# Performance work log

Measured on AMD Instinct MI355X. Metric: run time of the kernel, lower is better.

The kernel has to match this reference:

```python
import jax, jax.numpy as jnp
import numpy as np

N_NODES = 50000
N_EDGES = 800000
IN_DIM = 128
EDGE_DIM = 128
OUT_DIM = 128
N_AGG = 4          # mean, max, min, std
N_SCALE = 3        # identity, amplification, attenuation
AVG_D_LOG = float(np.log(17.0))  # log(avg_degree + 1), PNA avg_d['log']
EPS = 1e-5


def setup_inputs() -> dict:
    key = jax.random.key(0)
    ks = jax.random.split(key, 10)
    pre_in = 2 * IN_DIM + EDGE_DIM                      # pretrans input dim
    post_in = (N_AGG * N_SCALE + 1) * IN_DIM            # posttrans input dim
    return {
        "node_feat": jax.random.normal(ks[0], (N_NODES, IN_DIM), jnp.float32),
        "edge_feat": jax.random.normal(ks[1], (N_EDGES, EDGE_DIM), jnp.float32),
        "w_pre": jax.random.normal(ks[2], (pre_in, IN_DIM), jnp.float32) * (1.0 / np.sqrt(pre_in)),
        "b_pre": jnp.zeros((IN_DIM,), jnp.float32),
        "w_post1": jax.random.normal(ks[3], (post_in, OUT_DIM), jnp.float32) * (1.0 / np.sqrt(post_in)),
        "b_post1": jnp.zeros((OUT_DIM,), jnp.float32),
        "w_post2": jax.random.normal(ks[4], (OUT_DIM, OUT_DIM), jnp.float32) * (1.0 / np.sqrt(OUT_DIM)),
        "b_post2": jnp.zeros((OUT_DIM,), jnp.float32),
        "src": jax.random.randint(ks[5], (N_EDGES,), 0, N_NODES, jnp.int32),
        "dst": jax.random.randint(ks[6], (N_EDGES,), 0, N_NODES, jnp.int32),
    }


def reference(node_feat, edge_feat, w_pre, b_pre, w_post1, b_post1,
              w_post2, b_post2, src, dst):
    n = node_feat.shape[0]
    # --- pretrans over edges: MLP(cat[src_h, dst_h, edge_feat]) -> message ---
    z = jnp.concatenate([node_feat[src], node_feat[dst], edge_feat], axis=-1)  # [E, 2d+de]
    msg = jax.nn.relu(z @ w_pre + b_pre)                                       # [E, d]

    # --- multi-aggregator scatter-reduce per destination node ---
    ones = jnp.ones((msg.shape[0],), msg.dtype)
    deg = jax.ops.segment_sum(ones, dst, num_segments=n)                       # [N]
    d_safe = jnp.maximum(deg, 1.0)[:, None]
    has_nb = (deg > 0)[:, None]

    s1 = jax.ops.segment_sum(msg, dst, num_segments=n)
    s2 = jax.ops.segment_sum(msg * msg, dst, num_segments=n)
    a_mean = s1 / d_safe
    a_var = jax.nn.relu(s2 / d_safe - a_mean * a_mean)
    a_std = jnp.sqrt(a_var + EPS)
    a_max = jnp.where(has_nb, jax.ops.segment_max(msg, dst, num_segments=n), 0.0)
    a_min = jnp.where(has_nb, jax.ops.segment_min(msg, dst, num_segments=n), 0.0)
    agg = jnp.concatenate([a_mean, a_max, a_min, a_std], axis=-1)              # [N, 4d]

    # --- degree scalers: identity, amplification, attenuation ---
    logd = jnp.log(deg + 1.0)[:, None]
    amp = agg * (logd / AVG_D_LOG)
    att = agg * (AVG_D_LOG / jnp.maximum(logd, EPS))
    h = jnp.concatenate([node_feat, agg, amp, att], axis=-1)                   # [N, 13d]

    # --- posttrans MLP + residual ---
    h1 = jax.nn.relu(h @ w_post1 + b_post1)
    out = h1 @ w_post2 + b_post2 + node_feat                                   # residual (in_dim == out_dim)
    return out
```

## Files before the change

### kernel.cpp

```cpp
#include <hip/hip_runtime.h>
#include <math.h>

#define N_NODES 50000
#define N_EDGES 800000
#define D 128
#define AVG_D_LOG 2.833213344056216f
#define EPS 1e-5f

typedef __attribute__((ext_vector_type(8))) short bf16x8;
typedef __attribute__((ext_vector_type(4))) float f32x4;

__device__ __forceinline__ unsigned short f2bf(float x) {
    unsigned u = __float_as_uint(x);
    u += 0x7fffu + ((u >> 16) & 1u);
    return (unsigned short)(u >> 16);
}
__device__ __forceinline__ unsigned pk2bf(float a, float b) {
    return (unsigned)f2bf(a) | ((unsigned)f2bf(b) << 16);
}
__device__ __forceinline__ float bf2f(unsigned short u) {
    return __uint_as_float(((unsigned)u) << 16);
}

__global__ void k_init(int* hist, float* s1, float* s2, float* mx, float* mn) {
    size_t stride = (size_t)gridDim.x * blockDim.x;
    size_t i0 = (size_t)blockIdx.x * blockDim.x + threadIdx.x;
    const size_t ND4 = (size_t)N_NODES * D / 4;
    float4 z4 = {0.f, 0.f, 0.f, 0.f};
    int4 inf4 = {0x7f800000, 0x7f800000, 0x7f800000, 0x7f800000};
    for (size_t t = i0; t < ND4; t += stride) {
        ((float4*)s1)[t] = z4; ((float4*)s2)[t] = z4; ((float4*)mx)[t] = z4;
        ((int4*)mn)[t] = inf4;
    }
    for (size_t t = i0; t < N_NODES; t += stride) hist[t] = 0;
}

__global__ void k_hist(const int* __restrict__ dst, int* hist) {
    int e = blockIdx.x * blockDim.x + threadIdx.x;
    if (e < N_EDGES) atomicAdd(&hist[dst[e]], 1);
}

__global__ void k_scan(const int* __restrict__ hist, int* cursor) {
    __shared__ int part[256];
    __shared__ int base_s[256];
    int t = threadIdx.x;
    const int chunk = (N_NODES + 255) / 256;
    int lo = t * chunk;
    int hi = lo + chunk; if (hi > N_NODES) hi = N_NODES;
    int s = 0;
    for (int i = lo; i < hi; ++i) s += hist[i];
    part[t] = s;
    __syncthreads();
    if (t == 0) {
        int run = 0;
        for (int i = 0; i < 256; ++i) { base_s[i] = run; run += part[i]; }
    }
    __syncthreads();
    int run = base_s[t];
    for (int i = lo; i < hi; ++i) { cursor[i] = run; run += hist[i]; }
}

__global__ void k_scatter(const int* __restrict__ dst, int* cursor, int* perm) {
    int e = blockIdx.x * blockDim.x + threadIdx.x;
    if (e < N_EDGES) {
        int pos = atomicAdd(&cursor[dst[e]], 1);
        perm[pos] = e;
    }
}

__global__ void k_prepT(const float* __restrict__ w, unsigned short* __restrict__ wT, int K) {
    int idx = blockIdx.x * blockDim.x + threadIdx.x;
    if (idx >= K * D) return;
    int k = idx >> 7, c = idx & 127;
    wT[(size_t)c * K + k] = f2bf(w[idx]);
}

__global__ __launch_bounds__(256) void k_pretrans(
    const float* __restrict__ nf, const float* __restrict__ ef,
    const unsigned short* __restrict__ wpT, const float* __restrict__ bp,
    const int* __restrict__ src, const int* __restrict__ dst,
    const int* __restrict__ perm,
    float* s1, float* s2, float* mx, float* mn)
{
    __shared__ __align__(16) char smem[24576];
    __shared__ int pidx[64], sidx[64], didx[64];
    __shared__ int seg_start[65], seg_dst[64];
    __shared__ int nseg_s;
    __shared__ float sb[128];

    int t = threadIdx.x;
    int e0 = blockIdx.x * 64;
    if (t < 64) {
        int pe = perm[e0 + t];
        pidx[t] = pe; sidx[t] = src[pe]; didx[t] = dst[pe];
    }
    if (t < 128) sb[t] = bp[t];
    __syncthreads();

    int w  = t >> 6;
    int l  = t & 63;
    int lr = l & 15;
    int lg = l >> 4;

    f32x4 acc[2][4];
    #pragma unroll
    for (int i = 0; i < 2; ++i)
        #pragma unroll
        for (int j = 0; j < 4; ++j) acc[i][j] = (f32x4){0.f, 0.f, 0.f, 0.f};

    uint4  pw0, pw1, pw2, pw3;
    float4 pz0, pz1, pz2, pz3;

#define ZROW(NC, e) ((NC) < 2 ? nf + (size_t)sidx[e] * D : \
                     (NC) < 4 ? nf + (size_t)didx[e] * D : \
                                ef + (size_t)pidx[e] * D)

#define PF(NC) do { \
    { int g = t;       int c = g >> 3, j = g & 7;  pw0 = *(const uint4*)(wpT + (size_t)c * 384 + (NC) * 64 + j * 8); } \
    { int g = t + 256; int c = g >> 3, j = g & 7;  pw1 = *(const uint4*)(wpT + (size_t)c * 384 + (NC) * 64 + j * 8); } \
    { int g = t + 512; int c = g >> 3, j = g & 7;  pw2 = *(const uint4*)(wpT + (size_t)c * 384 + (NC) * 64 + j * 8); } \
    { int g = t + 768; int c = g >> 3, j = g & 7;  pw3 = *(const uint4*)(wpT + (size_t)c * 384 + (NC) * 64 + j * 8); } \
    { int g = t;       int e = g >> 4, q = g & 15; pz0 = *(const float4*)(ZROW(NC, e) + (((NC) & 1) * 64) + q * 4); } \
    { int g = t + 256; int e = g >> 4, q = g & 15; pz1 = *(const float4*)(ZROW(NC, e) + (((NC) & 1) * 64) + q * 4); } \
    { int g = t + 512; int e = g >> 4, q = g & 15; pz2 = *(const float4*)(ZROW(NC, e) + (((NC) & 1) * 64) + q * 4); } \
    { int g = t + 768; int e = g >> 4, q = g & 15; pz3 = *(const float4*)(ZROW(NC, e) + (((NC) & 1) * 64) + q * 4); } \
} while (0)

#define WR() do { \
    { int g = t;       int c = g >> 3, j = g & 7;  *(uint4*)(smem + c * 128 + ((j * 16) ^ ((c & 7) << 4))) = pw0; } \
    { int g = t + 256; int c = g >> 3, j = g & 7;  *(uint4*)(smem + c * 128 + ((j * 16) ^ ((c & 7) << 4))) = pw1; } \
    { int g = t + 512; int c = g >> 3, j = g & 7;  *(uint4*)(smem + c * 128 + ((j * 16) ^ ((c & 7) << 4))) = pw2; } \
    { int g = t + 768; int c = g >> 3, j = g & 7;  *(uint4*)(smem + c * 128 + ((j * 16) ^ ((c & 7) << 4))) = pw3; } \
    { int g = t;       int e = g >> 4, q = g & 15; uint2 hv = { pk2bf(pz0.x, pz0.y), pk2bf(pz0.z, pz0.w) }; \
      *(uint2*)(smem + 16384 + e * 128 + ((q * 8) ^ ((e & 7) << 4))) = hv; } \
    { int g = t + 256; int e = g >> 4, q = g & 15; uint2 hv = { pk2bf(pz1.x, pz1.y), pk2bf(pz1.z, pz1.w) }; \
      *(uint2*)(smem + 16384 + e * 128 + ((q * 8) ^ ((e & 7) << 4))) = hv; } \
    { int g = t + 512; int e = g >> 4, q = g & 15; uint2 hv = { pk2bf(pz2.x, pz2.y), pk2bf(pz2.z, pz2.w) }; \
      *(uint2*)(smem + 16384 + e * 128 + ((q * 8) ^ ((e & 7) << 4))) = hv; } \
    { int g = t + 768; int e = g >> 4, q = g & 15; uint2 hv = { pk2bf(pz3.x, pz3.y), pk2bf(pz3.z, pz3.w) }; \
      *(uint2*)(smem + 16384 + e * 128 + ((q * 8) ^ ((e & 7) << 4))) = hv; } \
} while (0)

#define MM() do { \
    _Pragma("unroll") \
    for (int ks = 0; ks < 2; ++ks) { \
        bf16x8 afr[2], bfr[4]; \
        int kb = ks * 64 + lg * 16; \
        _Pragma("unroll") \
        for (int cf = 0; cf < 2; ++cf) { \
            int c = w * 32 + cf * 16 + lr; \
            afr[cf] = *(const bf16x8*)(smem + c * 128 + (kb ^ ((c & 7) << 4))); \
        } \
        _Pragma("unroll") \
        for (int eb = 0; eb < 4; ++eb) { \
            int e = eb * 16 + lr; \
            bfr[eb] = *(const bf16x8*)(smem + 16384 + e * 128 + (kb ^ ((e & 7) << 4))); \
        } \
        _Pragma("unroll") \
        for (int cf = 0; cf < 2; ++cf) \
            _Pragma("unroll") \
            for (int eb = 0; eb < 4; ++eb) \
                acc[cf][eb] = __builtin_amdgcn_mfma_f32_16x16x32_bf16( \
                    afr[cf], bfr[eb], acc[cf][eb], 0, 0, 0); \
    } \
} while (0)

    PF(0);
    WR(); PF(1); __syncthreads(); MM(); __syncthreads();
    WR(); PF(2); __syncthreads(); MM(); __syncthreads();
    WR(); PF(3); __syncthreads(); MM(); __syncthreads();
    WR(); PF(4); __syncthreads(); MM(); __syncthreads();
    WR(); PF(5); __syncthreads(); MM(); __syncthreads();
    WR();        __syncthreads(); MM(); __syncthreads();

#undef ZROW
#undef PF
#undef WR
#undef MM

    #pragma unroll
    for (int cf = 0; cf < 2; ++cf)
        #pragma unroll
        for (int eb = 0; eb < 4; ++eb) {
            int e  = eb * 16 + lr;
            int c0 = w * 32 + cf * 16 + lg * 4;
            float v0 = fmaxf(acc[cf][eb][0] + sb[c0 + 0], 0.f);
            float v1 = fmaxf(acc[cf][eb][1] + sb[c0 + 1], 0.f);
            float v2 = fmaxf(acc[cf][eb][2] + sb[c0 + 2], 0.f);
            float v3 = fmaxf(acc[cf][eb][3] + sb[c0 + 3], 0.f);
            uint2 mv = { pk2bf(v0, v1), pk2bf(v2, v3) };
            *(uint2*)(smem + e * 256 + ((c0 * 2) ^ ((e & 7) << 4))) = mv;
        }
    if (t == 0) {
        int ns = 0;
        for (int e = 0; e < 64; ++e) {
            if (e == 0 || didx[e] != didx[e - 1]) { seg_dst[ns] = didx[e]; seg_start[ns] = e; ++ns; }
        }
        seg_start[ns] = 64; nseg_s = ns;
    }
    __syncthreads();
    int nseg = nseg_s;
    for (int idx = t; idx < nseg * D; idx += 256) {
        int sg = idx >> 7, c = idx & 127;
        int eb2 = seg_start[sg], ee = seg_start[sg + 1];
        float s = 0.f, q = 0.f, vmax = 0.f, vmin = __int_as_float(0x7f800000);
        for (int e = eb2; e < ee; ++e) {
            float v = bf2f(*(const unsigned short*)(smem + e * 256 + ((c * 2) ^ ((e & 7) << 4))));
            s += v; q += v * v;
            vmax = fmaxf(vmax, v); vmin = fminf(vmin, v);
        }
        size_t base = (size_t)seg_dst[sg] * D + c;
        atomicAdd(&s1[base], s);
        atomicAdd(&s2[base], q);
        atomicMax((int*)&mx[base], __float_as_int(vmax));
        atomicMin((int*)&mn[base], __float_as_int(vmin));
    }
}

__global__ void k_finalize(float* s1, float* s2, float* mx, float* mn,
                           const int* __restrict__ hist, float* scal) {
    size_t idx = (size_t)blockIdx.x * blockDim.x + threadIdx.x;
    if (idx >= (size_t)N_NODES * D) return;
    int n = (int)(idx >> 7);
    int c = (int)(idx & 127);
    float dg = (float)hist[n];
    float ds = fmaxf(dg, 1.f);
    float m  = s1[idx] / ds;
    float var = fmaxf(s2[idx] / ds - m * m, 0.f);
    float sd  = sqrtf(var + EPS);
    bool nb = dg > 0.f;
    s1[idx] = m;
    mx[idx] = nb ? mx[idx] : 0.f;
    mn[idx] = nb ? mn[idx] : 0.f;
    s2[idx] = sd;
    if (c == 0) {
        float logd = logf(dg + 1.f);
        scal[2 * n]     = logd / AVG_D_LOG;
        scal[2 * n + 1] = AVG_D_LOG / fmaxf(logd, EPS);
    }
}

__global__ __launch_bounds__(256, 3) void k_post1(
    const float* __restrict__ nf,
    const float* __restrict__ amean, const float* __restrict__ amax,
    const float* __restrict__ amin,  const float* __restrict__ astd,
    const float* __restrict__ scal,
    const unsigned short* __restrict__ w1T, const float* __restrict__ b1,
    unsigned short* __restrict__ h1bf)
{
    __shared__ __align__(16) char smem[49152];
    __shared__ float samp[64], satt[64], sb[128];

    int t = threadIdx.x;
    int n0 = blockIdx.x * 64;
    if (t < 64) {
        int n = n0 + t;
        samp[t] = (n < N_NODES) ? scal[2 * n] : 0.f;
        satt[t] = (n < N_NODES) ? scal[2 * n + 1] : 0.f;
    }
    if (t < 128) sb[t] = b1[t];
    __syncthreads();

    int w  = t >> 6, l = t & 63, lr = l & 15, lg = l >> 4;
    f32x4 acc[2][4];
    #pragma unroll
    for (int i = 0; i < 2; ++i)
        #pragma unroll
        for (int j = 0; j < 4; ++j) acc[i][j] = (f32x4){0.f, 0.f, 0.f, 0.f};

    for (int chunk = 0; chunk < 13; ++chunk) {
        #pragma unroll
        for (int p = 0; p < 8; ++p) {
            int g = t + 256 * p;
            int c = g >> 4, j = g & 15;
            uint4 wv = *(const uint4*)(w1T + (size_t)c * 1664 + chunk * 128 + j * 8);
            *(uint4*)(smem + c * 256 + ((j * 16) ^ ((c & 7) << 4))) = wv;
        }
        const float* base;
        int r;
        if (chunk == 0) { base = nf; r = 0; }
        else {
            int b = (chunk - 1) & 3;
            r = (chunk - 1) >> 2;
            base = (b == 0) ? amean : (b == 1) ? amax : (b == 2) ? amin : astd;
        }
        #pragma unroll
        for (int p = 0; p < 8; ++p) {
            int g = t + 256 * p;
            int e = g >> 5, q = g & 31;
            int n = n0 + e;
            float4 fv = {0.f, 0.f, 0.f, 0.f};
            if (n < N_NODES) {
                fv = *(const float4*)(base + (size_t)n * D + q * 4);
                if (r == 1) { float sc = samp[e]; fv.x *= sc; fv.y *= sc; fv.z *= sc; fv.w *= sc; }
                else if (r == 2) { float sc = satt[e]; fv.x *= sc; fv.y *= sc; fv.z *= sc; fv.w *= sc; }
            }
            uint2 hv = { pk2bf(fv.x, fv.y), pk2bf(fv.z, fv.w) };
            *(uint2*)(smem + 32768 + e * 256 + ((q * 8) ^ ((e & 7) << 4))) = hv;
        }
        __syncthreads();
        #pragma unroll
        for (int ks = 0; ks < 4; ++ks) {
            bf16x8 afr[2], bfr[4];
            int kb = ks * 64 + lg * 16;
            #pragma unroll
            for (int cf = 0; cf < 2; ++cf) {
                int c = w * 32 + cf * 16 + lr;
                afr[cf] = *(const bf16x8*)(smem + c * 256 + (kb ^ ((c & 7) << 4)));
            }
            #pragma unroll
            for (int eb = 0; eb < 4; ++eb) {
                int e = eb * 16 + lr;
                bfr[eb] = *(const bf16x8*)(smem + 32768 + e * 256 + (kb ^ ((e & 7) << 4)));
            }
            #pragma unroll
            for (int cf = 0; cf < 2; ++cf)
                #pragma unroll
                for (int eb = 0; eb < 4; ++eb)
                    acc[cf][eb] = __builtin_amdgcn_mfma_f32_16x16x32_bf16(
                        afr[cf], bfr[eb], acc[cf][eb], 0, 0, 0);
        }
        __syncthreads();
    }

    #pragma unroll
    for (int cf = 0; cf < 2; ++cf)
        #pragma unroll
        for (int eb = 0; eb < 4; ++eb) {
            int n = n0 + eb * 16 + lr;
            if (n < N_NODES) {
                int c0 = w * 32 + cf * 16 + lg * 4;
                float v0 = fmaxf(acc[cf][eb][0] + sb[c0 + 0], 0.f);
                float v1 = fmaxf(acc[cf][eb][1] + sb[c0 + 1], 0.f);
                float v2 = fmaxf(acc[cf][eb][2] + sb[c0 + 2], 0.f);
                float v3 = fmaxf(acc[cf][eb][3] + sb[c0 + 3], 0.f);
                uint2 hv = { pk2bf(v0, v1), pk2bf(v2, v3) };
                *(uint2*)(h1bf + (size_t)n * D + c0) = hv;
            }
        }
}

__global__ __launch_bounds__(256, 3) void k_post2(
    const unsigned short* __restrict__ h1bf, const unsigned short* __restrict__ w2T,
    const float* __restrict__ b2, const float* __restrict__ nf,
    float* __restrict__ out)
{
    __shared__ __align__(16) char smem[49152];
    __shared__ float sb[128];

    int t = threadIdx.x;
    int n0 = blockIdx.x * 64;
    if (t < 128) sb[t] = b2[t];

    int w  = t >> 6, l = t & 63, lr = l & 15, lg = l >> 4;
    f32x4 acc[2][4];
    #pragma unroll
    for (int i = 0; i < 2; ++i)
        #pragma unroll
        for (int j = 0; j < 4; ++j) acc[i][j] = (f32x4){0.f, 0.f, 0.f, 0.f};

    #pragma unroll
    for (int p = 0; p < 8; ++p) {
        int g = t + 256 * p;
        int c = g >> 4, j = g & 15;
        uint4 wv = *(const uint4*)(w2T + (size_t)c * 128 + j * 8);
        *(uint4*)(smem + c * 256 + ((j * 16) ^ ((c & 7) << 4))) = wv;
    }
    #pragma unroll
    for (int p = 0; p < 4; ++p) {
        int g = t + 256 * p;
        int e = g >> 4, j = g & 15;
        int n = n0 + e;
        uint4 hv = {0u, 0u, 0u, 0u};
        if (n < N_NODES) hv = *(const uint4*)(h1bf + (size_t)n * D + j * 8);
        *(uint4*)(smem + 32768 + e * 256 + ((j * 16) ^ ((e & 7) << 4))) = hv;
    }
    __syncthreads();
    #pragma unroll
    for (int ks = 0; ks < 4; ++ks) {
        bf16x8 afr[2], bfr[4];
        int kb = ks * 64 + lg * 16;
        #pragma unroll
        for (int cf = 0; cf < 2; ++cf) {
            int c = w * 32 + cf * 16 + lr;
            afr[cf] = *(const bf16x8*)(smem + c * 256 + (kb ^ ((c & 7) << 4)));
        }
        #pragma unroll
        for (int eb = 0; eb < 4; ++eb) {
            int e = eb * 16 + lr;
            bfr[eb] = *(const bf16x8*)(smem + 32768 + e * 256 + (kb ^ ((e & 7) << 4)));
        }
        #pragma unroll
        for (int cf = 0; cf < 2; ++cf)
            #pragma unroll
            for (int eb = 0; eb < 4; ++eb)
                acc[cf][eb] = __builtin_amdgcn_mfma_f32_16x16x32_bf16(
                    afr[cf], bfr[eb], acc[cf][eb], 0, 0, 0);
    }

    #pragma unroll
    for (int cf = 0; cf < 2; ++cf)
        #pragma unroll
        for (int eb = 0; eb < 4; ++eb) {
            int n = n0 + eb * 16 + lr;
            if (n < N_NODES) {
                int c0 = w * 32 + cf * 16 + lg * 4;
                float4 rv = *(const float4*)(nf + (size_t)n * D + c0);
                float4 ov = { acc[cf][eb][0] + sb[c0 + 0] + rv.x,
                              acc[cf][eb][1] + sb[c0 + 1] + rv.y,
                              acc[cf][eb][2] + sb[c0 + 2] + rv.z,
                              acc[cf][eb][3] + sb[c0 + 3] + rv.w };
                *(float4*)(out + (size_t)n * D + c0) = ov;
            }
        }
}

extern "C" void kernel_launch(void* const* d_in, const int* in_sizes, int n_in,
                              void* d_out, int out_size, void* d_ws, size_t ws_size,
                              hipStream_t stream) {
    const float* nf = (const float*)d_in[0];
    const float* ef = (const float*)d_in[1];
    const float* wp = (const float*)d_in[2];
    const float* bp = (const float*)d_in[3];
    const float* w1 = (const float*)d_in[4];
    const float* b1 = (const float*)d_in[5];
    const float* w2 = (const float*)d_in[6];
    const float* b2 = (const float*)d_in[7];
    const int* src  = (const int*)d_in[8];
    const int* dst  = (const int*)d_in[9];
    float* out = (float*)d_out;

    const size_t ND = (size_t)N_NODES * D;
    float* ws     = (float*)d_ws;
    int*   hist   = (int*)ws;
    int*   cursor = hist + 50048;
    int*   perm   = cursor + 50048;
    unsigned short* wpT = (unsigned short*)(perm + N_EDGES);
    unsigned short* w1T = wpT + 49152;
    unsigned short* w2T = w1T + 212992;
    float* s1     = (float*)(w2T + 16384);
    float* s2     = s1 + ND;
    float* mx     = s2 + ND;
    float* mn     = mx + ND;
    float* scal   = mn + ND;
    unsigned short* h1bf = (unsigned short*)(scal + 100096);

    hipLaunchKernelGGL(k_init, dim3(2048), dim3(256), 0, stream, hist, s1, s2, mx, mn);
    hipLaunchKernelGGL(k_hist, dim3((N_EDGES + 255) / 256), dim3(256), 0, stream, dst, hist);
    hipLaunchKernelGGL(k_scan, dim3(1), dim3(256), 0, stream, hist, cursor);
    hipLaunchKernelGGL(k_scatter, dim3((N_EDGES + 255) / 256), dim3(256), 0, stream, dst, cursor, perm);
    hipLaunchKernelGGL(k_prepT, dim3(192), dim3(256), 0, stream, wp, wpT, 384);
    hipLaunchKernelGGL(k_prepT, dim3(832), dim3(256), 0, stream, w1, w1T, 1664);
    hipLaunchKernelGGL(k_prepT, dim3(64),  dim3(256), 0, stream, w2, w2T, 128);
    hipLaunchKernelGGL(k_pretrans, dim3(N_EDGES / 64), dim3(256), 0, stream,
                       nf, ef, wpT, bp, src, dst, perm, s1, s2, mx, mn);
    hipLaunchKernelGGL(k_finalize, dim3((unsigned)((ND + 255) / 256)), dim3(256), 0, stream,
                       s1, s2, mx, mn, hist, scal);
    hipLaunchKernelGGL(k_post1, dim3((N_NODES + 63) / 64), dim3(256), 0, stream,
                       nf, s1, mx, mn, s2, scal, w1T, b1, h1bf);
    hipLaunchKernelGGL(k_post2, dim3((N_NODES + 63) / 64), dim3(256), 0, stream,
                       h1bf, w2T, b2, nf, out);
}
```

Baseline: 608.8 us.

## Replace atomic scatter aggregation with CSR segmented reduction over stored messages

The pretrans kernel now writes bf16 messages, sorted by destination, to a global buffer instead of doing atomic segment reductions. A new per-node kernel walks each node's contiguous CSR range and computes sum, sum of squares, max, min and the degree scalers in one pass. This removes the float atomics, the large init of the s1/s2/mx/mn arrays and the separate finalize pass. In exchange it adds a write and re-read of a 200MB message buffer, and it falls back to the old path when the workspace is too small.

```diff
diff --git a/kernel.cpp b/kernel.cpp
--- a/kernel.cpp
+++ b/kernel.cpp
@@ -33,6 +33,11 @@
         ((int4*)mn)[t] = inf4;
     }
     for (size_t t = i0; t < N_NODES; t += stride) hist[t] = 0;
+}
+
+__global__ void k_init_h(int* hist) {
+    int i = blockIdx.x * blockDim.x + threadIdx.x;
+    if (i < N_NODES) hist[i] = 0;
 }
 
 __global__ void k_hist(const int* __restrict__ dst, int* hist) {
@@ -75,46 +80,9 @@
     wT[(size_t)c * K + k] = f2bf(w[idx]);
 }
 
-__global__ __launch_bounds__(256) void k_pretrans(
-    const float* __restrict__ nf, const float* __restrict__ ef,
-    const unsigned short* __restrict__ wpT, const float* __restrict__ bp,
-    const int* __restrict__ src, const int* __restrict__ dst,
-    const int* __restrict__ perm,
-    float* s1, float* s2, float* mx, float* mn)
-{
-    __shared__ __align__(16) char smem[24576];
-    __shared__ int pidx[64], sidx[64], didx[64];
-    __shared__ int seg_start[65], seg_dst[64];
-    __shared__ int nseg_s;
-    __shared__ float sb[128];
-
-    int t = threadIdx.x;
-    int e0 = blockIdx.x * 64;
-    if (t < 64) {
-        int pe = perm[e0 + t];
-        pidx[t] = pe; sidx[t] = src[pe]; didx[t] = dst[pe];
-    }
-    if (t < 128) sb[t] = bp[t];
-    __syncthreads();
-
-    int w  = t >> 6;
-    int l  = t & 63;
-    int lr = l & 15;
-    int lg = l >> 4;
-
-    f32x4 acc[2][4];
-    #pragma unroll
-    for (int i = 0; i < 2; ++i)
-        #pragma unroll
-        for (int j = 0; j < 4; ++j) acc[i][j] = (f32x4){0.f, 0.f, 0.f, 0.f};
-
-    uint4  pw0, pw1, pw2, pw3;
-    float4 pz0, pz1, pz2, pz3;
-
 #define ZROW(NC, e) ((NC) < 2 ? nf + (size_t)sidx[e] * D : \
                      (NC) < 4 ? nf + (size_t)didx[e] * D : \
                                 ef + (size_t)pidx[e] * D)
-
 #define PF(NC) do { \
     { int g = t;       int c = g >> 3, j = g & 7;  pw0 = *(const uint4*)(wpT + (size_t)c * 384 + (NC) * 64 + j * 8); } \
     { int g = t + 256; int c = g >> 3, j = g & 7;  pw1 = *(const uint4*)(wpT + (size_t)c * 384 + (NC) * 64 + j * 8); } \
@@ -125,7 +93,6 @@
     { int g = t + 512; int e = g >> 4, q = g & 15; pz2 = *(const float4*)(ZROW(NC, e) + (((NC) & 1) * 64) + q * 4); } \
     { int g = t + 768; int e = g >> 4, q = g & 15; pz3 = *(const float4*)(ZROW(NC, e) + (((NC) & 1) * 64) + q * 4); } \
 } while (0)
-
 #define WR() do { \
     { int g = t;       int c = g >> 3, j = g & 7;  *(uint4*)(smem + c * 128 + ((j * 16) ^ ((c & 7) << 4))) = pw0; } \
     { int g = t + 256; int c = g >> 3, j = g & 7;  *(uint4*)(smem + c * 128 + ((j * 16) ^ ((c & 7) << 4))) = pw1; } \
@@ -140,7 +107,6 @@
     { int g = t + 768; int e = g >> 4, q = g & 15; uint2 hv = { pk2bf(pz3.x, pz3.y), pk2bf(pz3.z, pz3.w) }; \
       *(uint2*)(smem + 16384 + e * 128 + ((q * 8) ^ ((e & 7) << 4))) = hv; } \
 } while (0)
-
 #define MM() do { \
     _Pragma("unroll") \
     for (int ks = 0; ks < 2; ++ks) { \
@@ -165,6 +131,40 @@
     } \
 } while (0)
 
+__global__ __launch_bounds__(256) void k_pretrans_g(
+    const float* __restrict__ nf, const float* __restrict__ ef,
+    const unsigned short* __restrict__ wpT, const float* __restrict__ bp,
+    const int* __restrict__ src, const int* __restrict__ dst,
+    const int* __restrict__ perm,
+    unsigned short* __restrict__ msgG)
+{
+    __shared__ __align__(16) char smem[24576];
+    __shared__ int pidx[64], sidx[64], didx[64];
+    __shared__ float sb[128];
+
+    int t = threadIdx.x;
+    int e0 = blockIdx.x * 64;
+    if (t < 64) {
+        int pe = perm[e0 + t];
+        pidx[t] = pe; sidx[t] = src[pe]; didx[t] = dst[pe];
+    }
+    if (t < 128) sb[t] = bp[t];
+    __syncthreads();
+
+    int w  = t >> 6;
+    int l  = t & 63;
+    int lr = l & 15;
+    int lg = l >> 4;
+
+    f32x4 acc[2][4];
+    #pragma unroll
+    for (int i = 0; i < 2; ++i)
+        #pragma unroll
+        for (int j = 0; j < 4; ++j) acc[i][j] = (f32x4){0.f, 0.f, 0.f, 0.f};
+
+    uint4  pw0, pw1, pw2, pw3;
+    float4 pz0, pz1, pz2, pz3;
+
     PF(0);
     WR(); PF(1); __syncthreads(); MM(); __syncthreads();
     WR(); PF(2); __syncthreads(); MM(); __syncthreads();
@@ -172,11 +172,6 @@
     WR(); PF(4); __syncthreads(); MM(); __syncthreads();
     WR(); PF(5); __syncthreads(); MM(); __syncthreads();
     WR();        __syncthreads(); MM(); __syncthreads();
-
-#undef ZROW
-#undef PF
-#undef WR
-#undef MM
 
     #pragma unroll
     for (int cf = 0; cf < 2; ++cf)
@@ -191,6 +186,117 @@
             uint2 mv = { pk2bf(v0, v1), pk2bf(v2, v3) };
             *(uint2*)(smem + e * 256 + ((c0 * 2) ^ ((e & 7) << 4))) = mv;
         }
+    __syncthreads();
+    #pragma unroll
+    for (int p = 0; p < 4; ++p) {
+        int e = (t >> 4) + p * 16;
+        int q = t & 15;
+        uint4 v = *(const uint4*)(smem + e * 256 + q * 16);
+        int qq = q ^ (e & 7);
+        *(uint4*)(msgG + (size_t)(e0 + e) * D + qq * 8) = v;
+    }
+}
+
+__global__ __launch_bounds__(256) void k_agg(
+    const unsigned short* __restrict__ msgG,
+    const int* __restrict__ cursor, const int* __restrict__ hist,
+    float* __restrict__ s1, float* __restrict__ s2,
+    float* __restrict__ mx, float* __restrict__ mn, float* __restrict__ scal)
+{
+    int t = threadIdx.x;
+    int n = blockIdx.x * 4 + (t >> 6);
+    int tl = t & 63;
+    int deg = hist[n];
+    int re  = cursor[n];
+    int rs  = re - deg;
+
+    float sum0 = 0.f, sum1 = 0.f, sq0 = 0.f, sq1 = 0.f;
+    float mx0 = -3.402823e38f, mx1 = -3.402823e38f;
+    float mn0 =  3.402823e38f, mn1 =  3.402823e38f;
+    const uint* mg = (const uint*)msgG;
+    for (int e = 0; e < deg; ++e) {
+        uint v = mg[(size_t)(rs + e) * 64 + tl];
+        float a = bf2f((unsigned short)(v & 0xffff));
+        float b = bf2f((unsigned short)(v >> 16));
+        sum0 += a; sum1 += b; sq0 += a * a; sq1 += b * b;
+        mx0 = fmaxf(mx0, a); mx1 = fmaxf(mx1, b);
+        mn0 = fminf(mn0, a); mn1 = fminf(mn1, b);
+    }
+    float dg = (float)deg;
+    float ds = fmaxf(dg, 1.f);
+    bool nb = deg > 0;
+    float m0 = sum0 / ds, m1 = sum1 / ds;
+    float sd0 = sqrtf(fmaxf(sq0 / ds - m0 * m0, 0.f) + EPS);
+    float sd1 = sqrtf(fmaxf(sq1 / ds - m1 * m1, 0.f) + EPS);
+    size_t base = (size_t)n * D + tl * 2;
+    *(float2*)&s1[base] = (float2){m0, m1};
+    *(float2*)&s2[base] = (float2){sd0, sd1};
+    *(float2*)&mx[base] = (float2){nb ? mx0 : 0.f, nb ? mx1 : 0.f};
+    *(float2*)&mn[base] = (float2){nb ? mn0 : 0.f, nb ? mn1 : 0.f};
+    if (tl == 0) {
+        float logd = logf(dg + 1.f);
+        scal[2 * n]     = logd / AVG_D_LOG;
+        scal[2 * n + 1] = AVG_D_LOG / fmaxf(logd, EPS);
+    }
+}
+
+__global__ __launch_bounds__(256) void k_pretrans(
+    const float* __restrict__ nf, const float* __restrict__ ef,
+    const unsigned short* __restrict__ wpT, const float* __restrict__ bp,
+    const int* __restrict__ src, const int* __restrict__ dst,
+    const int* __restrict__ perm,
+    float* s1, float* s2, float* mx, float* mn)
+{
+    __shared__ __align__(16) char smem[24576];
+    __shared__ int pidx[64], sidx[64], didx[64];
+    __shared__ int seg_start[65], seg_dst[64];
+    __shared__ int nseg_s;
+    __shared__ float sb[128];
+
+    int t = threadIdx.x;
+    int e0 = blockIdx.x * 64;
+    if (t < 64) {
+        int pe = perm[e0 + t];
+        pidx[t] = pe; sidx[t] = src[pe]; didx[t] = dst[pe];
+    }
+    if (t < 128) sb[t] = bp[t];
+    __syncthreads();
+
+    int w  = t >> 6;
+    int l  = t & 63;
+    int lr = l & 15;
+    int lg = l >> 4;
+
+    f32x4 acc[2][4];
+    #pragma unroll
+    for (int i = 0; i < 2; ++i)
+        #pragma unroll
+        for (int j = 0; j < 4; ++j) acc[i][j] = (f32x4){0.f, 0.f, 0.f, 0.f};
+
+    uint4  pw0, pw1, pw2, pw3;
+    float4 pz0, pz1, pz2, pz3;
+
+    PF(0);
+    WR(); PF(1); __syncthreads(); MM(); __syncthreads();
+    WR(); PF(2); __syncthreads(); MM(); __syncthreads();
+    WR(); PF(3); __syncthreads(); MM(); __syncthreads();
+    WR(); PF(4); __syncthreads(); MM(); __syncthreads();
+    WR(); PF(5); __syncthreads(); MM(); __syncthreads();
+    WR();        __syncthreads(); MM(); __syncthreads();
+
+    #pragma unroll
+    for (int cf = 0; cf < 2; ++cf)
+        #pragma unroll
+        for (int eb = 0; eb < 4; ++eb) {
+            int e  = eb * 16 + lr;
+            int c0 = w * 32 + cf * 16 + lg * 4;
+            float v0 = fmaxf(acc[cf][eb][0] + sb[c0 + 0], 0.f);
+            float v1 = fmaxf(acc[cf][eb][1] + sb[c0 + 1], 0.f);
+            float v2 = fmaxf(acc[cf][eb][2] + sb[c0 + 2], 0.f);
+            float v3 = fmaxf(acc[cf][eb][3] + sb[c0 + 3], 0.f);
+            uint2 mv = { pk2bf(v0, v1), pk2bf(v2, v3) };
+            *(uint2*)(smem + e * 256 + ((c0 * 2) ^ ((e & 7) << 4))) = mv;
+        }
     if (t == 0) {
         int ns = 0;
         for (int e = 0; e < 64; ++e) {
@@ -216,6 +322,11 @@
         atomicMin((int*)&mn[base], __float_as_int(vmin));
     }
 }
+
+#undef ZROW
+#undef PF
+#undef WR
+#undef MM
 
 __global__ void k_finalize(float* s1, float* s2, float* mx, float* mn,
                            const int* __restrict__ hist, float* scal) {
@@ -431,31 +542,55 @@
     float* out = (float*)d_out;
 
     const size_t ND = (size_t)N_NODES * D;
-    float* ws     = (float*)d_ws;
-    int*   hist   = (int*)ws;
+    char* wsb = (char*)d_ws;
+    int*   hist   = (int*)wsb;
     int*   cursor = hist + 50048;
     int*   perm   = cursor + 50048;
     unsigned short* wpT = (unsigned short*)(perm + N_EDGES);
     unsigned short* w1T = wpT + 49152;
     unsigned short* w2T = w1T + 212992;
-    float* s1     = (float*)(w2T + 16384);
+    unsigned short* msgG = w2T + 16384;
+    const size_t MSG_SH = (size_t)N_EDGES * D;
+    float* s1     = (float*)(msgG + MSG_SH);
     float* s2     = s1 + ND;
     float* mx     = s2 + ND;
     float* mn     = mx + ND;
     float* scal   = mn + ND;
     unsigned short* h1bf = (unsigned short*)(scal + 100096);
-
-    hipLaunchKernelGGL(k_init, dim3(2048), dim3(256), 0, stream, hist, s1, s2, mx, mn);
+    size_t need_csr = (size_t)((char*)(h1bf + ND) - wsb);
+
+    bool use_csr = ws_size >= need_csr;
+    if (!use_csr) {
+        s1   = (float*)(w2T + 16384);
+        s2   = s1 + ND;
+        mx   = s2 + ND;
+        mn   = mx + ND;
+        scal = mn + ND;
+        h1bf = (unsigned short*)(scal + 100096);
+    }
+
+    if (use_csr) {
+        hipLaunchKernelGGL(k_init_h, dim3((N_NODES + 255) / 256), dim3(256), 0, stream, hist);
+    } else {
+        hipLaunchKernelGGL(k_init, dim3(2048), dim3(256), 0, stream, hist, s1, s2, mx, mn);
+    }
     hipLaunchKernelGGL(k_hist, dim3((N_EDGES + 255) / 256), dim3(256), 0, stream, dst, hist);
     hipLaunchKernelGGL(k_scan, dim3(1), dim3(256), 0, stream, hist, cursor);
     hipLaunchKernelGGL(k_scatter, dim3((N_EDGES + 255) / 256), dim3(256), 0, stream, dst, cursor, perm);
     hipLaunchKernelGGL(k_prepT, dim3(192), dim3(256), 0, stream, wp, wpT, 384);
     hipLaunchKernelGGL(k_prepT, dim3(832), dim3(256), 0, stream, w1, w1T, 1664);
     hipLaunchKernelGGL(k_prepT, dim3(64),  dim3(256), 0, stream, w2, w2T, 128);
-    hipLaunchKernelGGL(k_pretrans, dim3(N_EDGES / 64), dim3(256), 0, stream,
-                       nf, ef, wpT, bp, src, dst, perm, s1, s2, mx, mn);
-    hipLaunchKernelGGL(k_finalize, dim3((unsigned)((ND + 255) / 256)), dim3(256), 0, stream,
-                       s1, s2, mx, mn, hist, scal);
+    if (use_csr) {
+        hipLaunchKernelGGL(k_pretrans_g, dim3(N_EDGES / 64), dim3(256), 0, stream,
+                           nf, ef, wpT, bp, src, dst, perm, msgG);
+        hipLaunchKernelGGL(k_agg, dim3(N_NODES / 4), dim3(256), 0, stream,
+                           msgG, cursor, hist, s1, s2, mx, mn, scal);
+    } else {
+        hipLaunchKernelGGL(k_pretrans, dim3(N_EDGES / 64), dim3(256), 0, stream,
+                           nf, ef, wpT, bp, src, dst, perm, s1, s2, mx, mn);
+        hipLaunchKernelGGL(k_finalize, dim3((unsigned)((ND + 255) / 256)), dim3(256), 0, stream,
+                           s1, s2, mx, mn, hist, scal);
+    }
     hipLaunchKernelGGL(k_post1, dim3((N_NODES + 63) / 64), dim3(256), 0, stream,
                        nf, s1, mx, mn, s2, scal, w1T, b1, h1bf);
     hipLaunchKernelGGL(k_post2, dim3((N_NODES + 63) / 64), dim3(256), 0, stream,
```

New measurement: 611.9 us. No clear change (+0.5%).
